# Kernel optimization log

Measured on AMD Instinct MI355X. Metric: run time of the kernel, lower is better.

## Reference

```python
import jax, jax.numpy as jnp
import numpy as np

ALPHA = -10.0  # softmax sharpness on |x - bin| distances
TAU = 0.0
TAU2 = 0.0
EPS = 1e-10

B, F, L, K = 32, 64, 1024, 32


def setup_inputs() -> dict:
    key = jax.random.key(0)
    k1, k2 = jax.random.split(key)
    x = jax.random.normal(k1, (B, F, L), dtype=jnp.float32)
    bins = jax.random.normal(k2, (K,), dtype=jnp.float32)
    return {"x": x, "bins": bins}


def reference(x, bins):
    # dist: [B, F, L, K] = |x[..., None] - bins|
    dist = jnp.abs(x[..., None] - bins)
    # soft assignment over the K bins (training path of the module)
    soft = jax.nn.softmax(ALPHA * dist, axis=-1)
    assignment = soft + EPS

    # weighted quantization loss: sum of per-bin mean of sqrt(assignment)
    quant = jnp.sum(jnp.mean(jnp.sqrt(assignment), axis=(0, 1, 2)))
    weighted_quant_loss = jnp.stack([quant, jnp.float32(TAU2)])[None, :]  # [1, 2]

    # code entropy of average assignment distribution
    p = jnp.mean(assignment, axis=(0, 1, 2))  # [K]
    code_entropy = -jnp.sum(p * jnp.log(p))
    weighted_code_entropy = jnp.stack([code_entropy, jnp.float32(TAU)])[None, :]  # [1, 2]

    # soft reconstruction against the bins: [B, F, L]
    bit_code = jnp.einsum('bflk,k->bfl', assignment, bins)
    return bit_code, weighted_code_entropy, weighted_quant_loss
```

## Files before the change

kernel.cpp:

```cpp
#include <hip/hip_runtime.h>

#define K      32
#define KQ     8
#define TPB    256
#define NB     4096
#define EPT    8
#define NTOT   (32 * 64 * 1024)
#define PSTRIDE (NB * (TPB / 4))

__device__ __forceinline__ float wave_reduce_sum(float v) {
#pragma unroll
  for (int m = 1; m < 64; m <<= 1) v += __shfl_xor(v, m, 64);
  return v;
}

__device__ __forceinline__ float quarter_reduce(float v) {
#pragma unroll
  for (int m = 4; m < 64; m <<= 1) v += __shfl_xor(v, m, 64);
  return v;
}

__global__ __launch_bounds__(TPB)
void ssq_main(const float* __restrict__ x, const float* __restrict__ bins,
              float* __restrict__ out, float* __restrict__ partials) {
  const int tid     = threadIdx.x;
  const int quarter = tid & 3;
  const int pslot   = blockIdx.x * (TPB / 4) + (tid >> 2);

  float binv[KQ];
#pragma unroll
  for (int j = 0; j < KQ; ++j) binv[j] = bins[KQ * quarter + j];
  float bs = 0.f;
#pragma unroll
  for (int j = 0; j < KQ; ++j) bs += binv[j];
  bs += __shfl_xor(bs, 1, 64);
  bs += __shfl_xor(bs, 2, 64);
  const float epsb = 1e-10f * bs;

  float xs[EPT];
#pragma unroll
  for (int e = 0; e < EPT; ++e) xs[e] = x[pslot + e * PSTRIDE];

  float sAcc[KQ];
#pragma unroll
  for (int j = 0; j < KQ; ++j) sAcc[j] = 0.f;
  float q = 0.f;

  const float Ch = -7.213475204444817f;

#pragma unroll 1
  for (int e = 0; e < EPT; ++e) {
    const float xv = xs[e];
    float t[KQ];
    float s0 = 0.f, s1 = 0.f, h0 = 0.f, h1 = 0.f, b0 = 0.f, b1 = 0.f;
#pragma unroll
    for (int j = 0; j < KQ; j += 2) {
      float ha = __builtin_amdgcn_exp2f(Ch * fabsf(xv - binv[j + 0]));
      float hb = __builtin_amdgcn_exp2f(Ch * fabsf(xv - binv[j + 1]));
      float ta = ha * ha, tb = hb * hb;
      t[j + 0] = ta; t[j + 1] = tb;
      s0 += ta; s1 += tb;
      h0 += ha; h1 += hb;
      b0 = fmaf(ta, binv[j + 0], b0);
      b1 = fmaf(tb, binv[j + 1], b1);
    }
    float s_loc = s0 + s1, b_loc = b0 + b1;
    float s2 = s_loc + __shfl_xor(s_loc, 1, 64);
    float b2 = b_loc + __shfl_xor(b_loc, 1, 64);
    const float s_full = s2 + __shfl_xor(s2, 2, 64);
    const float b_full = b2 + __shfl_xor(b2, 2, 64);
    const float inv = __builtin_amdgcn_rcpf(s_full);
    q = fmaf(h0 + h1, __builtin_amdgcn_rsqf(s_full), q);
    if (quarter == 0) out[pslot + e * PSTRIDE] = fmaf(b_full, inv, epsb);
#pragma unroll
    for (int j = 0; j < KQ; ++j) sAcc[j] = fmaf(t[j], inv, sAcc[j]);
  }

  __shared__ float red[4][K + 1];
  const int lane = tid & 63, wv = tid >> 6;
#pragma unroll
  for (int j = 0; j < KQ; ++j) {
    float v = quarter_reduce(sAcc[j]);
    if (lane < 4) red[wv][KQ * lane + j] = v;
  }
  {
    float v = wave_reduce_sum(q);
    if (lane == 0) red[wv][K] = v;
  }
  __syncthreads();
  if (tid < K + 1) {
    float v = red[0][tid] + red[1][tid] + red[2][tid] + red[3][tid];
    partials[tid * NB + blockIdx.x] = v;
  }
}

__global__ __launch_bounds__(1024)
void ssq_tail(const float* __restrict__ partials, float* __restrict__ out) {
  const int tid = threadIdx.x, lane = tid & 63, wv = tid >> 6;
  __shared__ float sums[K + 1];
  for (int c = wv; c < K + 1; c += 16) {
    const float* p = partials + c * NB;
    float s = 0.f;
#pragma unroll
    for (int j = 0; j < NB / 64; ++j) s += p[lane + j * 64];
    s = wave_reduce_sum(s);
    if (lane == 0) sums[c] = s;
  }
  __syncthreads();
  if (wv == 0) {
    float e = 0.f;
    if (lane < K) {
      float p = sums[lane] * (1.0f / (float)NTOT) + 1e-10f;
      e = -p * __logf(p);
    }
    e = wave_reduce_sum(e);
    if (lane == 0) {
      out[NTOT + 0] = e;
      out[NTOT + 1] = 0.f;
      out[NTOT + 2] = sums[K] * (1.0f / (float)NTOT);
      out[NTOT + 3] = 0.f;
    }
  }
}

extern "C" void kernel_launch(void* const* d_in, const int* in_sizes, int n_in,
                              void* d_out, int out_size, void* d_ws, size_t ws_size,
                              hipStream_t stream) {
  const float* x    = (const float*)d_in[0];
  const float* bins = (const float*)d_in[1];
  float* out        = (float*)d_out;
  float* partials   = (float*)d_ws;

  ssq_main<<<NB, TPB,  0, stream>>>(x, bins, out, partials);
  ssq_tail<<<1,  1024, 0, stream>>>(partials, out);
}
```

Measured before the change: 87.46 us.

## Use DPP quad shuffles and split tail reduction across parallel blocks

Replaces the xor-1/xor-2 lane shuffles inside the hot loop with DPP quad-permute operations, which avoid LDS-routed ds_bpermute traffic. It also replaces the single-block tail reduction with a 33-block parallel reduction followed by a tiny final kernel that computes entropy and the quant loss. This trades one extra kernel launch for more parallelism in reducing the partials.

```diff
diff --git a/kernel.cpp b/kernel.cpp
--- a/kernel.cpp
+++ b/kernel.cpp
@@ -12,6 +12,15 @@
 #pragma unroll
   for (int m = 1; m < 64; m <<= 1) v += __shfl_xor(v, m, 64);
   return v;
+}
+
+__device__ __forceinline__ float dpp_xor1(float v) {
+  return __int_as_float(__builtin_amdgcn_update_dpp(
+      0, __float_as_int(v), 0xB1, 0xF, 0xF, true));
+}
+__device__ __forceinline__ float dpp_xor2(float v) {
+  return __int_as_float(__builtin_amdgcn_update_dpp(
+      0, __float_as_int(v), 0x4E, 0xF, 0xF, true));
 }
 
 __device__ __forceinline__ float quarter_reduce(float v) {
@@ -33,8 +42,8 @@
   float bs = 0.f;
 #pragma unroll
   for (int j = 0; j < KQ; ++j) bs += binv[j];
-  bs += __shfl_xor(bs, 1, 64);
-  bs += __shfl_xor(bs, 2, 64);
+  bs += dpp_xor1(bs);
+  bs += dpp_xor2(bs);
   const float epsb = 1e-10f * bs;
 
   float xs[EPT];
@@ -65,10 +74,10 @@
       b1 = fmaf(tb, binv[j + 1], b1);
     }
     float s_loc = s0 + s1, b_loc = b0 + b1;
-    float s2 = s_loc + __shfl_xor(s_loc, 1, 64);
-    float b2 = b_loc + __shfl_xor(b_loc, 1, 64);
-    const float s_full = s2 + __shfl_xor(s2, 2, 64);
-    const float b_full = b2 + __shfl_xor(b2, 2, 64);
+    float s2 = s_loc + dpp_xor1(s_loc);
+    float b2 = b_loc + dpp_xor1(b_loc);
+    const float s_full = s2 + dpp_xor2(s2);
+    const float b_full = b2 + dpp_xor2(b2);
     const float inv = __builtin_amdgcn_rcpf(s_full);
     q = fmaf(h0 + h1, __builtin_amdgcn_rsqf(s_full), q);
     if (quarter == 0) out[pslot + e * PSTRIDE] = fmaf(b_full, inv, epsb);
@@ -94,32 +103,33 @@
   }
 }
 
-__global__ __launch_bounds__(1024)
-void ssq_tail(const float* __restrict__ partials, float* __restrict__ out) {
-  const int tid = threadIdx.x, lane = tid & 63, wv = tid >> 6;
-  __shared__ float sums[K + 1];
-  for (int c = wv; c < K + 1; c += 16) {
-    const float* p = partials + c * NB;
-    float s = 0.f;
+__global__ __launch_bounds__(TPB)
+void ssq_reduce(const float* __restrict__ partials, float* __restrict__ sums) {
+  const float* p = partials + blockIdx.x * NB;
+  const int tid  = threadIdx.x;
+  float s = 0.f;
 #pragma unroll
-    for (int j = 0; j < NB / 64; ++j) s += p[lane + j * 64];
-    s = wave_reduce_sum(s);
-    if (lane == 0) sums[c] = s;
+  for (int j = 0; j < NB / TPB; ++j) s += p[tid + j * TPB];
+  s = wave_reduce_sum(s);
+  __shared__ float red[4];
+  if ((tid & 63) == 0) red[tid >> 6] = s;
+  __syncthreads();
+  if (tid == 0) sums[blockIdx.x] = red[0] + red[1] + red[2] + red[3];
+}
+
+__global__ void ssq_final(const float* __restrict__ sums, float* __restrict__ out) {
+  const int lane = threadIdx.x;
+  float e = 0.f;
+  if (lane < K) {
+    float p = sums[lane] * (1.0f / (float)NTOT) + 1e-10f;
+    e = -p * __logf(p);
   }
-  __syncthreads();
-  if (wv == 0) {
-    float e = 0.f;
-    if (lane < K) {
-      float p = sums[lane] * (1.0f / (float)NTOT) + 1e-10f;
-      e = -p * __logf(p);
-    }
-    e = wave_reduce_sum(e);
-    if (lane == 0) {
-      out[NTOT + 0] = e;
-      out[NTOT + 1] = 0.f;
-      out[NTOT + 2] = sums[K] * (1.0f / (float)NTOT);
-      out[NTOT + 3] = 0.f;
-    }
+  e = wave_reduce_sum(e);
+  if (lane == 0) {
+    out[NTOT + 0] = e;
+    out[NTOT + 1] = 0.f;
+    out[NTOT + 2] = sums[K] * (1.0f / (float)NTOT);
+    out[NTOT + 3] = 0.f;
   }
 }
 
@@ -130,7 +140,9 @@
   const float* bins = (const float*)d_in[1];
   float* out        = (float*)d_out;
   float* partials   = (float*)d_ws;
+  float* sums       = partials + (K + 1) * NB;
 
-  ssq_main<<<NB, TPB,  0, stream>>>(x, bins, out, partials);
-  ssq_tail<<<1,  1024, 0, stream>>>(partials, out);
+  ssq_main  <<<NB,    TPB, 0, stream>>>(x, bins, out, partials);
+  ssq_reduce<<<K + 1, TPB, 0, stream>>>(partials, sums);
+  ssq_final <<<1,     64,  0, stream>>>(sums, out);
 }
```

Result: no change. 86.07 us (-1.6%).
